# Kernel optimization log

Hardware: AMD Instinct MI355X
Metric: run time of the kernel (lower is better)

## Reference

```python
import jax, jax.numpy as jnp
import numpy as np
from jax import lax

T, Nn, K, IN, H1, H2, G, P, HEADS = 64, 2048, 32, 256, 128, 128, 256, 60, 3


def setup_inputs() -> dict:
    key = jax.random.key(0)
    ks = jax.random.split(key, 20)
    s = 0.05  # weight scale to keep activations sane
    return {
        'h': jax.random.normal(ks[0], (T, Nn, IN), jnp.float32),
        'neigh': jax.random.randint(ks[1], (Nn, K), 0, Nn),
        'Npop': jnp.ones((1,), jnp.float32) * 1e6,
        'I': jax.random.uniform(ks[2], (T,), jnp.float32) * 1e4,
        'R': jax.random.uniform(ks[3], (T,), jnp.float32) * 1e4,
        'S': jax.random.uniform(ks[4], (T,), jnp.float32) * 9e5,
        'It': jax.random.uniform(ks[5], (T,), jnp.float32),
        'Rt': jax.random.uniform(ks[6], (T,), jnp.float32),
        'fc1': jax.random.normal(ks[7], (HEADS, IN, H1), jnp.float32) * s,
        'fc2': jax.random.normal(ks[8], (HEADS * H1, H2), jnp.float32) * s,
        'gru_Wih': jax.random.normal(ks[9], (3 * G, H2), jnp.float32) * s,
        'gru_Whh': jax.random.normal(ks[10], (3 * G, G), jnp.float32) * s,
        'gru_bih': jax.random.normal(ks[11], (3 * G,), jnp.float32) * s,
        'gru_bhh': jax.random.normal(ks[12], (3 * G,), jnp.float32) * s,
        'res1_W': jax.random.normal(ks[13], (2 * P, G + 2), jnp.float32) * s,
        'res1_b': jax.random.normal(ks[14], (2 * P,), jnp.float32) * s,
        'res2_W': jax.random.normal(ks[15], (2, G + 2), jnp.float32) * s,
        'res2_b': jax.random.normal(ks[16], (2,), jnp.float32) * s,
        'hx0': jax.random.normal(ks[17], (G,), jnp.float32),
    }


def _input_attention(iz, neigh):
    # cosine^4 edge scores, unnormalized weighted sum of neighbor feats
    src = iz[neigh]                                  # [N,K,d]
    dot = jnp.einsum('nkd,nd->nk', src, iz)
    nsrc = jnp.sqrt(jnp.einsum('nkd,nkd->nk', src, src))
    ndst = jnp.sqrt(jnp.sum(iz * iz, axis=-1))[:, None]
    e = (dot / nsrc / ndst) ** 4                     # [N,K]
    return jnp.einsum('nk,nkd->nd', e, src)


def _gat_head(x, W, neigh):
    # dot-product edge attention + per-node softmax + weighted reduce
    z = x @ W                                        # [N,H]
    src = z[neigh]                                   # [N,K,H]
    e = jnp.einsum('nkd,nd->nk', src, z)             # [N,K]
    a = jax.nn.softmax(e, axis=1)
    return jnp.einsum('nk,nkd->nd', a, src)


def _gru_cell(x, hx, Wih, Whh, bih, bhh):
    gi = Wih @ x + bih                               # [3G]
    gh = Whh @ hx + bhh
    ir, iz, inn = jnp.split(gi, 3)
    hr, hz, hn = jnp.split(gh, 3)
    r = jax.nn.sigmoid(ir + hr)
    zg = jax.nn.sigmoid(iz + hz)
    n = jnp.tanh(inn + r * hn)
    return (1.0 - zg) * n + zg * hx


def reference(h, neigh, Npop, I, R, S, It, Rt, fc1, fc2, gru_Wih, gru_Whh,
              gru_bih, gru_bhh, res1_W, res1_b, res2_W, res2_b, hx0):
    Np = Npop[0]

    def step(hx, xs):
        h_t, I_t, R_t, S_t, It_t, Rt_t = xs
        ih = _input_attention(h_t, neigh)                       # [N,in]
        heads = jax.vmap(lambda W: _gat_head(ih, W, neigh))(fc1)  # [3,N,H1]
        c = jax.nn.relu(jnp.transpose(heads, (1, 0, 2)).reshape(Nn, HEADS * H1))
        c = _gat_head(c, fc2, neigh)                            # [N,H2]
        pooled = jnp.max(jax.nn.relu(c), axis=0)                # [H2]
        hx = _gru_cell(pooled, hx, gru_Wih, gru_Whh, gru_bih, gru_bhh)
        nhx = jnp.concatenate([hx, It_t[None], Rt_t[None]])     # [G+2]
        pred = res1_W @ nhx + res1_b                            # [2P]
        ab = res2_W @ nhx + res2_b
        a_s = jax.nn.sigmoid(ab[0])
        b_s = jax.nn.sigmoid(ab[1])
        new_I = pred[0::2]
        new_R = pred[1::2]

        def sir(st, _):
            lI, lR, lS = st
            dI = a_s * lI * (lS / Np) - b_s * lI
            dR = b_s * lI
            nI = lI + lax.stop_gradient(dI)
            nR = lR + lax.stop_gradient(dR)
            nS = Np - nI - nR
            return (nI, nR, nS), (dI, dR)

        _, (pI, pR) = lax.scan(sir, (I_t, R_t, S_t), None, length=P)
        return hx, (new_I, new_R, pI, pR)

    _, (new_I, new_R, phy_I, phy_R) = lax.scan(step, hx0, (h, I, R, S, It, Rt))
    return (new_I, new_R, phy_I.reshape(-1), phy_R.reshape(-1))
```

## Files before the change

### kernel.cpp

```cpp
#include <hip/hip_runtime.h>
#include <hip/hip_bf16.h>
#include <math.h>

#define T_STEPS 64
#define NN      2048
#define KN      32
#define IND     256
#define H1D     128
#define C1D     384
#define H2D     128
#define GD      256
#define PD      60
#define GRU_NB  8

#define BITREV5_INIT {0,16,8,24,4,20,12,28,2,18,10,26,6,22,14,30, \
                      1,17,9,25,5,21,13,29,3,19,11,27,7,23,15,31}

__device__ __forceinline__ float bcast_lane(float v, int lane_imm) {
    return __uint_as_float(__builtin_amdgcn_readlane(__float_as_uint(v), lane_imm));
}

__device__ __forceinline__ float xpose_reduce16(float part[16], int lane) {
#pragma unroll
    for (int i = 0; i < 8; ++i) {
        float send = (lane & 2) ? part[i] : part[i + 8];
        float keep = (lane & 2) ? part[i + 8] : part[i];
        part[i] = keep + __shfl_xor(send, 2);
    }
#pragma unroll
    for (int i = 0; i < 4; ++i) {
        float send = (lane & 4) ? part[i] : part[i + 4];
        float keep = (lane & 4) ? part[i + 4] : part[i];
        part[i] = keep + __shfl_xor(send, 4);
    }
#pragma unroll
    for (int i = 0; i < 2; ++i) {
        float send = (lane & 8) ? part[i] : part[i + 2];
        float keep = (lane & 8) ? part[i + 2] : part[i];
        part[i] = keep + __shfl_xor(send, 8);
    }
    {
        float send = (lane & 16) ? part[0] : part[1];
        float keep = (lane & 16) ? part[1] : part[0];
        part[0] = keep + __shfl_xor(send, 16);
    }
    return part[0] + __shfl_xor(part[0], 32);
}

__global__ __launch_bounds__(256) void norms_kernel(const float* __restrict__ h,
                                                    float* __restrict__ norms,
                                                    int t_base) {
    int gw   = (int)((blockIdx.x * blockDim.x + threadIdx.x) >> 6);
    int lane = threadIdx.x & 63;
    int n    = gw & (NN - 1);
    int tloc = gw >> 11;
    const float4* row = (const float4*)(h + ((size_t)(t_base + tloc) * NN + n) * IND);
    float4 v = row[lane];
    float s = v.x * v.x + v.y * v.y + v.z * v.z + v.w * v.w;
#pragma unroll
    for (int off = 32; off > 0; off >>= 1) s += __shfl_xor(s, off);
    if (lane == 0) norms[(size_t)tloc * NN + n] = sqrtf(s);
}

__global__ __launch_bounds__(256, 4) void input_attn_kernel(const float* __restrict__ h,
                                                            const int* __restrict__ neigh,
                                                            const float* __restrict__ norms,
                                                            float* __restrict__ ih,
                                                            int t_base) {
    const int BR[32] = BITREV5_INIT;
    __shared__ float hd_s[2][2][32];
    int wave    = threadIdx.x >> 6;
    int nodeloc = wave >> 1;
    int half    = wave & 1;
    int lane    = threadIdx.x & 63;
    int gw   = (int)((blockIdx.x << 1) | nodeloc);
    int n    = gw & (NN - 1);
    int tloc = gw >> 11;
    const float* hT  = h + (size_t)(t_base + tloc) * NN * IND;
    const float* nrm = norms + (size_t)tloc * NN;

    const float2* dst2 = (const float2*)(hT + (size_t)n * IND + half * 128);
    float2 d = dst2[lane];

    int   jreg = neigh[n * KN + (lane & 31)];
    float nj   = nrm[jreg];
    float ndst = nrm[n];

    float2 rr[32];
    float comb[16];
#pragma unroll
    for (int i = 0; i < 16; ++i) {
        int sja = __builtin_amdgcn_readlane(jreg, BR[i]);
        int sjb = __builtin_amdgcn_readlane(jreg, BR[i + 16]);
        const float2* sa = (const float2*)(hT + (size_t)sja * IND + half * 128);
        const float2* sb = (const float2*)(hT + (size_t)sjb * IND + half * 128);
        rr[i]      = sa[lane];
        rr[i + 16] = sb[lane];
        float pa = rr[i].x * d.x + rr[i].y * d.y;
        float pb = rr[i + 16].x * d.x + rr[i + 16].y * d.y;
        float send = (lane & 1) ? pa : pb;
        float keep = (lane & 1) ? pb : pa;
        comb[i] = keep + __shfl_xor(send, 1);
    }
#pragma unroll
    for (int i = 0; i < 32; ++i) asm volatile("" : "+v"(rr[i].x), "+v"(rr[i].y));
    float hdot = xpose_reduce16(comb, lane);
    if (lane < 32) hd_s[nodeloc][half][lane] = hdot;
    __syncthreads();
    float dot = hdot + hd_s[nodeloc][half ^ 1][lane & 31];

    float r  = dot / (nj * ndst);
    float r2 = r * r;
    float e  = r2 * r2;

    float a0 = 0.f, a1 = 0.f;
#pragma unroll
    for (int i = 0; i < 32; ++i) {
        float ek = bcast_lane(e, BR[i]);
        a0 += ek * rr[i].x;
        a1 += ek * rr[i].y;
    }
    float2* orow = (float2*)(ih + (size_t)gw * IND + half * 128);
    orow[lane] = make_float2(a0, a1);
}

__global__ __launch_bounds__(256) void matmul_f32(const float* __restrict__ A,
                                                  const float* __restrict__ B,
                                                  float* __restrict__ C,
                                                  int M, int N, int K) {
    __shared__ float As[16][65];
    __shared__ float Bs[16][68];
    int tid  = threadIdx.x;
    int row0 = blockIdx.y * 64;
    int col0 = blockIdx.x * 64;
    int tr = tid >> 4, tc = tid & 15;
    float acc[4][4] = {};
    int la_m = tid >> 2;
    int la_k = (tid & 3) * 4;
    int lb_k = tid >> 4;
    int lb_n = (tid & 15) * 4;
    for (int k0 = 0; k0 < K; k0 += 16) {
        float4 av = *(const float4*)(A + (size_t)(row0 + la_m) * K + k0 + la_k);
        float4 bv = *(const float4*)(B + (size_t)(k0 + lb_k) * N + col0 + lb_n);
        __syncthreads();
        As[la_k + 0][la_m] = av.x; As[la_k + 1][la_m] = av.y;
        As[la_k + 2][la_m] = av.z; As[la_k + 3][la_m] = av.w;
        *(float4*)&Bs[lb_k][lb_n] = bv;
        __syncthreads();
#pragma unroll
        for (int kk = 0; kk < 16; ++kk) {
            float a[4], b[4];
#pragma unroll
            for (int r = 0; r < 4; ++r) a[r] = As[kk][tr * 4 + r];
#pragma unroll
            for (int c = 0; c < 4; ++c) b[c] = Bs[kk][tc * 4 + c];
#pragma unroll
            for (int r = 0; r < 4; ++r)
#pragma unroll
                for (int c = 0; c < 4; ++c) acc[r][c] += a[r] * b[c];
        }
    }
#pragma unroll
    for (int r = 0; r < 4; ++r) {
        float4 v = { acc[r][0], acc[r][1], acc[r][2], acc[r][3] };
        *(float4*)(C + (size_t)(row0 + tr * 4 + r) * N + col0 + tc * 4) = v;
    }
}

__global__ __launch_bounds__(192, 4) void gat_heads_kernel(const float* __restrict__ z1,
                                                           const int* __restrict__ neigh,
                                                           float* __restrict__ c) {
    const int BR[32] = BITREV5_INIT;
    int n    = blockIdx.x & (NN - 1);
    const float* ztbl = z1 + (size_t)(blockIdx.x >> 11) * NN * C1D;
    int head = threadIdx.x >> 6;
    int lane = threadIdx.x & 63;

    const float2* dst2 = (const float2*)(ztbl + (size_t)n * C1D + head * H1D);
    float2 d = dst2[lane];
    int jreg = neigh[n * KN + (lane & 31)];

    float2 rr[32];
    float comb[16];
#pragma unroll
    for (int i = 0; i < 16; ++i) {
        int sja = __builtin_amdgcn_readlane(jreg, BR[i]);
        int sjb = __builtin_amdgcn_readlane(jreg, BR[i + 16]);
        const float2* sa = (const float2*)(ztbl + (size_t)sja * C1D + head * H1D);
        const float2* sb = (const float2*)(ztbl + (size_t)sjb * C1D + head * H1D);
        rr[i]      = sa[lane];
        rr[i + 16] = sb[lane];
        float pa = rr[i].x * d.x + rr[i].y * d.y;
        float pb = rr[i + 16].x * d.x + rr[i + 16].y * d.y;
        float send = (lane & 1) ? pa : pb;
        float keep = (lane & 1) ? pb : pa;
        comb[i] = keep + __shfl_xor(send, 1);
    }
#pragma unroll
    for (int i = 0; i < 32; ++i) asm volatile("" : "+v"(rr[i].x), "+v"(rr[i].y));
    float dot = xpose_reduce16(comb, lane);

    float m = dot;
#pragma unroll
    for (int off = 16; off > 0; off >>= 1) m = fmaxf(m, __shfl_xor(m, off));
    float p = __expf(dot - m);
    float s = p;
#pragma unroll
    for (int off = 16; off > 0; off >>= 1) s += __shfl_xor(s, off);
    p /= s;

    float a0 = 0.f, a1 = 0.f;
#pragma unroll
    for (int i = 0; i < 32; ++i) {
        float pk = bcast_lane(p, BR[i]);
        a0 += pk * rr[i].x;
        a1 += pk * rr[i].y;
    }
    float2* orow = (float2*)(c + (size_t)blockIdx.x * C1D + (size_t)head * H1D);
    orow[lane] = make_float2(fmaxf(a0, 0.f), fmaxf(a1, 0.f));
}

__global__ __launch_bounds__(256, 4) void gat_final_kernel(const float* __restrict__ z2,
                                                           const int* __restrict__ neigh,
                                                           float* __restrict__ pooled,
                                                           int t_base) {
    const int BR[32] = BITREV5_INIT;
    __shared__ float2 red_s[4][64];
    int wave = threadIdx.x >> 6;
    int gw   = (int)((blockIdx.x << 2) | wave);
    int n    = gw & (NN - 1);
    int tloc = gw >> 11;
    const float* ztbl = z2 + (size_t)tloc * NN * H2D;
    int lane = threadIdx.x & 63;

    const float2* dst2 = (const float2*)(ztbl + (size_t)n * H2D);
    float2 d = dst2[lane];
    int jreg = neigh[n * KN + (lane & 31)];

    float2 rr[32];
    float comb[16];
#pragma unroll
    for (int i = 0; i < 16; ++i) {
        int sja = __builtin_amdgcn_readlane(jreg, BR[i]);
        int sjb = __builtin_amdgcn_readlane(jreg, BR[i + 16]);
        const float2* sa = (const float2*)(ztbl + (size_t)sja * H2D);
        const float2* sb = (const float2*)(ztbl + (size_t)sjb * H2D);
        rr[i]      = sa[lane];
        rr[i + 16] = sb[lane];
        float pa = rr[i].x * d.x + rr[i].y * d.y;
        float pb = rr[i + 16].x * d.x + rr[i + 16].y * d.y;
        float send = (lane & 1) ? pa : pb;
        float keep = (lane & 1) ? pb : pa;
        comb[i] = keep + __shfl_xor(send, 1);
    }
#pragma unroll
    for (int i = 0; i < 32; ++i) asm volatile("" : "+v"(rr[i].x), "+v"(rr[i].y));
    float dot = xpose_reduce16(comb, lane);

    float m = dot;
#pragma unroll
    for (int off = 16; off > 0; off >>= 1) m = fmaxf(m, __shfl_xor(m, off));
    float p = __expf(dot - m);
    float s = p;
#pragma unroll
    for (int off = 16; off > 0; off >>= 1) s += __shfl_xor(s, off);
    p /= s;

    float a0 = 0.f, a1 = 0.f;
#pragma unroll
    for (int i = 0; i < 32; ++i) {
        float pk = bcast_lane(p, BR[i]);
        a0 += pk * rr[i].x;
        a1 += pk * rr[i].y;
    }
    red_s[wave][lane] = make_float2(fmaxf(a0, 0.f), fmaxf(a1, 0.f));
    __syncthreads();
    if (wave == 0) {
        float mx0 = red_s[0][lane].x, mx1 = red_s[0][lane].y;
#pragma unroll
        for (int q = 1; q < 4; ++q) {
            mx0 = fmaxf(mx0, red_s[q][lane].x);
            mx1 = fmaxf(mx1, red_s[q][lane].y);
        }
        int* dst = (int*)(pooled + (size_t)(t_base + tloc) * H2D + lane * 2);
        atomicMax(dst,     __float_as_int(mx0));
        atomicMax(dst + 1, __float_as_int(mx1));
    }
}

__global__ void prep_W1(const float* __restrict__ fc1, float* __restrict__ W1,
                        unsigned int* __restrict__ cnt,
                        float* __restrict__ pooled) {
    int i = blockIdx.x * 256 + threadIdx.x;
    if (i < 256 * 384) {
        int d = i / 384, cf = i % 384;
        int hd = cf >> 7, j = cf & 127;
        W1[i] = fc1[(size_t)hd * 256 * 128 + (size_t)d * 128 + j];
    }
    if (i < T_STEPS) cnt[i] = 0u;
    if (i < T_STEPS * H2D) pooled[i] = 0.f;
}

__global__ __launch_bounds__(256) void gi_all_kernel(const float* __restrict__ Wih,
                                                     const float* __restrict__ bih,
                                                     const float* __restrict__ pooled,
                                                     float* __restrict__ gi_all) {
    __shared__ float p_s[H2D];
    int t  = blockIdx.x / 3;
    int ob = (blockIdx.x % 3) * 256;
    if (threadIdx.x < H2D) p_s[threadIdx.x] = pooled[t * H2D + threadIdx.x];
    __syncthreads();
    int o = ob + threadIdx.x;
    float acc = bih[o];
    const float* wr = Wih + (size_t)o * H2D;
#pragma unroll 4
    for (int d = 0; d < H2D; ++d) acc += wr[d] * p_s[d];
    gi_all[t * 768 + o] = acc;
}

__global__ __launch_bounds__(768) void gru_reg_kernel(const float* __restrict__ Whh,
                                                      const float* __restrict__ bhh,
                                                      const float* __restrict__ gi_all,
                                                      const float* __restrict__ hx0,
                                                      float* hx_all,
                                                      unsigned int* cnt) {
    __shared__ float4 hx_pad[72];
    __shared__ __align__(16) float hx_lin[GD];
    __shared__ float gh_s[96];
    int b   = blockIdx.x;
    int tid = threadIdx.x;
    int row_local = tid >> 3;
    int sub       = tid & 7;
    int chunk     = row_local >> 5;
    int r_in      = row_local & 31;
    int grow      = chunk * GD + b * 32 + r_in;

    float4 wreg[8];
    const float4* wrow = (const float4*)(Whh + (size_t)grow * GD + sub * 32);
#pragma unroll
    for (int i = 0; i < 8; ++i) wreg[i] = wrow[i];
    float bias = (sub == 0) ? bhh[grow] : 0.f;

    for (int t = 0; t < T_STEPS; ++t) {
        if (t > 0) {
            if (tid == 0) {
                while (__hip_atomic_load(&cnt[t - 1], __ATOMIC_ACQUIRE,
                                         __HIP_MEMORY_SCOPE_AGENT) < GRU_NB)
                    __builtin_amdgcn_s_sleep(1);
            }
            __syncthreads();
        }
        const float* hsrc = (t == 0) ? hx0 : (hx_all + (size_t)(t - 1) * GD);
        if (tid < 64) {
            float4 v;
            v.x = __hip_atomic_load(hsrc + tid * 4 + 0, __ATOMIC_RELAXED, __HIP_MEMORY_SCOPE_AGENT);
            v.y = __hip_atomic_load(hsrc + tid * 4 + 1, __ATOMIC_RELAXED, __HIP_MEMORY_SCOPE_AGENT);
            v.z = __hip_atomic_load(hsrc + tid * 4 + 2, __ATOMIC_RELAXED, __HIP_MEMORY_SCOPE_AGENT);
            v.w = __hip_atomic_load(hsrc + tid * 4 + 3, __ATOMIC_RELAXED, __HIP_MEMORY_SCOPE_AGENT);
            hx_pad[(tid >> 3) * 9 + (tid & 7)] = v;
            ((float4*)hx_lin)[tid] = v;
        }
        __syncthreads();

        float acc = 0.f;
#pragma unroll
        for (int i = 0; i < 8; ++i) {
            float4 hv = hx_pad[sub * 9 + i];
            float4 wv = wreg[i];
            acc += wv.x * hv.x + wv.y * hv.y + wv.z * hv.z + wv.w * hv.w;
        }
        acc += __shfl_xor(acc, 1);
        acc += __shfl_xor(acc, 2);
        acc += __shfl_xor(acc, 4);
        if (sub == 0) gh_s[row_local] = acc + bias;
        __syncthreads();

        if (tid < 32) {
            int u = b * 32 + tid;
            float gi_r = gi_all[t * 768 + u];
            float gi_z = gi_all[t * 768 + 256 + u];
            float gi_n = gi_all[t * 768 + 512 + u];
            float r  = 1.f / (1.f + expf(-(gi_r + gh_s[tid])));
            float zg = 1.f / (1.f + expf(-(gi_z + gh_s[32 + tid])));
            float nn = tanhf(gi_n + r * gh_s[64 + tid]);
            float hnew = (1.f - zg) * nn + zg * hx_lin[u];
            __hip_atomic_store(&hx_all[(size_t)t * GD + u], hnew,
                               __ATOMIC_RELAXED, __HIP_MEMORY_SCOPE_AGENT);
            __threadfence();
        }
        __syncthreads();
        if (tid == 0)
            __hip_atomic_fetch_add(&cnt[t], 1u, __ATOMIC_RELEASE,
                                   __HIP_MEMORY_SCOPE_AGENT);
    }
}

__global__ __launch_bounds__(128) void res_sir_kernel(const float* __restrict__ hx_all,
                                                      const float* __restrict__ It,
                                                      const float* __restrict__ Rt,
                                                      const float* __restrict__ r1W,
                                                      const float* __restrict__ r1b,
                                                      const float* __restrict__ r2W,
                                                      const float* __restrict__ r2b,
                                                      const float* __restrict__ I,
                                                      const float* __restrict__ R,
                                                      const float* __restrict__ S,
                                                      const float* __restrict__ Npop,
                                                      float* __restrict__ out) {
    __shared__ float nhx[258];
    __shared__ float ab_s[2];
    int t = blockIdx.x, tid = threadIdx.x;
    for (int i = tid; i < GD; i += 128) nhx[i] = hx_all[t * GD + i];
    if (tid == 0) { nhx[256] = It[t]; nhx[257] = Rt[t]; }
    __syncthreads();
    if (tid < 120) {
        float acc = r1b[tid];
        const float* wr = r1W + tid * 258;
        for (int d = 0; d < 258; ++d) acc += wr[d] * nhx[d];
        int idx = t * 60 + (tid >> 1);
        if (tid & 1) out[3840 + idx] = acc;
        else         out[idx] = acc;
    }
    if (tid == 120 || tid == 121) {
        int q = tid - 120;
        float acc = r2b[q];
        const float* wr = r2W + q * 258;
        for (int d = 0; d < 258; ++d) acc += wr[d] * nhx[d];
        ab_s[q] = acc;
    }
    __syncthreads();
    if (tid == 0) {
        float a_s = 1.f / (1.f + expf(-ab_s[0]));
        float b_s = 1.f / (1.f + expf(-ab_s[1]));
        float Np = Npop[0];
        float lI = I[t], lR = R[t], lS = S[t];
        for (int p = 0; p < PD; ++p) {
            float dI = a_s * lI * (lS / Np) - b_s * lI;
            float dR = b_s * lI;
            lI += dI;
            lR += dR;
            lS = Np - lI - lR;
            out[7680  + t * 60 + p] = dI;
            out[11520 + t * 60 + p] = dR;
        }
    }
}

extern "C" void kernel_launch(void* const* d_in, const int* in_sizes, int n_in,
                              void* d_out, int out_size, void* d_ws, size_t ws_size,
                              hipStream_t stream) {
    const float* h    = (const float*)d_in[0];
    const int*   ng   = (const int*)  d_in[1];
    const float* Npop = (const float*)d_in[2];
    const float* I_   = (const float*)d_in[3];
    const float* R_   = (const float*)d_in[4];
    const float* S_   = (const float*)d_in[5];
    const float* It   = (const float*)d_in[6];
    const float* Rt   = (const float*)d_in[7];
    const float* fc1  = (const float*)d_in[8];
    const float* fc2  = (const float*)d_in[9];
    const float* gWih = (const float*)d_in[10];
    const float* gWhh = (const float*)d_in[11];
    const float* gbih = (const float*)d_in[12];
    const float* gbhh = (const float*)d_in[13];
    const float* r1W  = (const float*)d_in[14];
    const float* r1b  = (const float*)d_in[15];
    const float* r2W  = (const float*)d_in[16];
    const float* r2b  = (const float*)d_in[17];
    const float* hx0  = (const float*)d_in[18];
    float* out = (float*)d_out;

    char* w = (char*)d_ws;
    float* pooled = (float*)w; w += (size_t)T_STEPS * H2D * 4;
    float* hx_all = (float*)w; w += (size_t)T_STEPS * GD * 4;
    float* W1     = (float*)w; w += (size_t)256 * 384 * 4;
    float* gi_all = (float*)w; w += (size_t)T_STEPS * 768 * 4;
    unsigned int* cnt = (unsigned int*)w; w += 256;
    size_t fixed = (size_t)(w - (char*)d_ws);

    int Tc = 16;
    while (Tc > 1) {
        size_t need = fixed + (size_t)Tc * (8192 + 2ull * 2048 * 384 * 4);
        if (need <= ws_size) break;
        Tc >>= 1;
    }
    float* norms = (float*)w; w += (size_t)Tc * NN * 4;
    float* bufA  = (float*)w; w += (size_t)Tc * NN * C1D * 4;
    float* bufB  = (float*)w;

    prep_W1<<<(256 * 384 + 255) / 256, 256, 0, stream>>>(fc1, W1, cnt, pooled);

    for (int t0 = 0; t0 < T_STEPS; t0 += Tc) {
        int M = Tc * NN;
        norms_kernel      <<<Tc * NN / 4, 256, 0, stream>>>(h, norms, t0);
        input_attn_kernel <<<Tc * NN / 2, 256, 0, stream>>>(h, ng, norms, bufA, t0);
        matmul_f32<<<dim3(384 / 64, M / 64), 256, 0, stream>>>(bufA, W1, bufB, M, 384, 256);
        gat_heads_kernel  <<<Tc * NN, 192, 0, stream>>>(bufB, ng, bufA);
        matmul_f32<<<dim3(128 / 64, M / 64), 256, 0, stream>>>(bufA, fc2, bufB, M, 128, 384);
        gat_final_kernel  <<<Tc * NN / 4, 256, 0, stream>>>(bufB, ng, pooled, t0);
    }

    gi_all_kernel<<<T_STEPS * 3, 256, 0, stream>>>(gWih, gbih, pooled, gi_all);
    gru_reg_kernel<<<GRU_NB, 768, 0, stream>>>(gWhh, gbhh, gi_all, hx0, hx_all, cnt);
    res_sir_kernel<<<T_STEPS, 128, 0, stream>>>(hx_all, It, Rt, r1W, r1b, r2W, r2b,
                                                I_, R_, S_, Npop, out);
}
```

Before: 1.774 ms.

## Replace atomic max pooling with two-stage reduction and batch gather loads

```diff
diff --git a/kernel.cpp b/kernel.cpp
--- a/kernel.cpp
+++ b/kernel.cpp
@@ -87,23 +87,23 @@
     float ndst = nrm[n];
 
     float2 rr[32];
+#pragma unroll
+    for (int i = 0; i < 32; ++i) {
+        int sj = __builtin_amdgcn_readlane(jreg, BR[i]);
+        rr[i] = ((const float2*)(hT + (size_t)sj * IND + half * 128))[lane];
+    }
+#pragma unroll
+    for (int i = 0; i < 32; ++i) asm volatile("" : "+v"(rr[i].x), "+v"(rr[i].y));
+
     float comb[16];
 #pragma unroll
     for (int i = 0; i < 16; ++i) {
-        int sja = __builtin_amdgcn_readlane(jreg, BR[i]);
-        int sjb = __builtin_amdgcn_readlane(jreg, BR[i + 16]);
-        const float2* sa = (const float2*)(hT + (size_t)sja * IND + half * 128);
-        const float2* sb = (const float2*)(hT + (size_t)sjb * IND + half * 128);
-        rr[i]      = sa[lane];
-        rr[i + 16] = sb[lane];
         float pa = rr[i].x * d.x + rr[i].y * d.y;
         float pb = rr[i + 16].x * d.x + rr[i + 16].y * d.y;
         float send = (lane & 1) ? pa : pb;
         float keep = (lane & 1) ? pb : pa;
         comb[i] = keep + __shfl_xor(send, 1);
     }
-#pragma unroll
-    for (int i = 0; i < 32; ++i) asm volatile("" : "+v"(rr[i].x), "+v"(rr[i].y));
     float hdot = xpose_reduce16(comb, lane);
     if (lane < 32) hd_s[nodeloc][half][lane] = hdot;
     __syncthreads();
@@ -181,23 +181,23 @@
     int jreg = neigh[n * KN + (lane & 31)];
 
     float2 rr[32];
+#pragma unroll
+    for (int i = 0; i < 32; ++i) {
+        int sj = __builtin_amdgcn_readlane(jreg, BR[i]);
+        rr[i] = ((const float2*)(ztbl + (size_t)sj * C1D + head * H1D))[lane];
+    }
+#pragma unroll
+    for (int i = 0; i < 32; ++i) asm volatile("" : "+v"(rr[i].x), "+v"(rr[i].y));
+
     float comb[16];
 #pragma unroll
     for (int i = 0; i < 16; ++i) {
-        int sja = __builtin_amdgcn_readlane(jreg, BR[i]);
-        int sjb = __builtin_amdgcn_readlane(jreg, BR[i + 16]);
-        const float2* sa = (const float2*)(ztbl + (size_t)sja * C1D + head * H1D);
-        const float2* sb = (const float2*)(ztbl + (size_t)sjb * C1D + head * H1D);
-        rr[i]      = sa[lane];
-        rr[i + 16] = sb[lane];
         float pa = rr[i].x * d.x + rr[i].y * d.y;
         float pb = rr[i + 16].x * d.x + rr[i + 16].y * d.y;
         float send = (lane & 1) ? pa : pb;
         float keep = (lane & 1) ? pb : pa;
         comb[i] = keep + __shfl_xor(send, 1);
     }
-#pragma unroll
-    for (int i = 0; i < 32; ++i) asm volatile("" : "+v"(rr[i].x), "+v"(rr[i].y));
     float dot = xpose_reduce16(comb, lane);
 
     float m = dot;
@@ -222,15 +222,11 @@
 
 __global__ __launch_bounds__(256, 4) void gat_final_kernel(const float* __restrict__ z2,
                                                            const int* __restrict__ neigh,
-                                                           float* __restrict__ pooled,
-                                                           int t_base) {
+                                                           float* __restrict__ c2) {
     const int BR[32] = BITREV5_INIT;
-    __shared__ float2 red_s[4][64];
-    int wave = threadIdx.x >> 6;
-    int gw   = (int)((blockIdx.x << 2) | wave);
+    int gw   = (int)((blockIdx.x << 2) | (threadIdx.x >> 6));
     int n    = gw & (NN - 1);
-    int tloc = gw >> 11;
-    const float* ztbl = z2 + (size_t)tloc * NN * H2D;
+    const float* ztbl = z2 + (size_t)(gw >> 11) * NN * H2D;
     int lane = threadIdx.x & 63;
 
     const float2* dst2 = (const float2*)(ztbl + (size_t)n * H2D);
@@ -238,23 +234,23 @@
     int jreg = neigh[n * KN + (lane & 31)];
 
     float2 rr[32];
+#pragma unroll
+    for (int i = 0; i < 32; ++i) {
+        int sj = __builtin_amdgcn_readlane(jreg, BR[i]);
+        rr[i] = ((const float2*)(ztbl + (size_t)sj * H2D))[lane];
+    }
+#pragma unroll
+    for (int i = 0; i < 32; ++i) asm volatile("" : "+v"(rr[i].x), "+v"(rr[i].y));
+
     float comb[16];
 #pragma unroll
     for (int i = 0; i < 16; ++i) {
-        int sja = __builtin_amdgcn_readlane(jreg, BR[i]);
-        int sjb = __builtin_amdgcn_readlane(jreg, BR[i + 16]);
-        const float2* sa = (const float2*)(ztbl + (size_t)sja * H2D);
-        const float2* sb = (const float2*)(ztbl + (size_t)sjb * H2D);
-        rr[i]      = sa[lane];
-        rr[i + 16] = sb[lane];
         float pa = rr[i].x * d.x + rr[i].y * d.y;
         float pb = rr[i + 16].x * d.x + rr[i + 16].y * d.y;
         float send = (lane & 1) ? pa : pb;
         float keep = (lane & 1) ? pb : pa;
         comb[i] = keep + __shfl_xor(send, 1);
     }
-#pragma unroll
-    for (int i = 0; i < 32; ++i) asm volatile("" : "+v"(rr[i].x), "+v"(rr[i].y));
     float dot = xpose_reduce16(comb, lane);
 
     float m = dot;
@@ -273,24 +269,33 @@
         a0 += pk * rr[i].x;
         a1 += pk * rr[i].y;
     }
-    red_s[wave][lane] = make_float2(fmaxf(a0, 0.f), fmaxf(a1, 0.f));
-    __syncthreads();
-    if (wave == 0) {
-        float mx0 = red_s[0][lane].x, mx1 = red_s[0][lane].y;
-#pragma unroll
-        for (int q = 1; q < 4; ++q) {
-            mx0 = fmaxf(mx0, red_s[q][lane].x);
-            mx1 = fmaxf(mx1, red_s[q][lane].y);
-        }
-        int* dst = (int*)(pooled + (size_t)(t_base + tloc) * H2D + lane * 2);
-        atomicMax(dst,     __float_as_int(mx0));
-        atomicMax(dst + 1, __float_as_int(mx1));
-    }
+    float2* orow = (float2*)(c2 + (size_t)gw * H2D);
+    orow[lane] = make_float2(fmaxf(a0, 0.f), fmaxf(a1, 0.f));
+}
+
+__global__ __launch_bounds__(128) void pool_part_kernel(const float* __restrict__ c2,
+                                                        float* __restrict__ ppart) {
+    int j = threadIdx.x;
+    int tloc  = blockIdx.x >> 4;
+    int slice = blockIdx.x & 15;
+    const float* base = c2 + ((size_t)tloc * NN + slice * 128) * H2D;
+    float mx = 0.f;
+    for (int q = 0; q < 128; ++q) mx = fmaxf(mx, base[(size_t)q * H2D + j]);
+    ppart[(size_t)blockIdx.x * H2D + j] = mx;
+}
+__global__ __launch_bounds__(128) void pool_reduce_kernel(const float* __restrict__ ppart,
+                                                          float* __restrict__ pooled,
+                                                          int t_base) {
+    int j = threadIdx.x;
+    const float* base = ppart + (size_t)blockIdx.x * 16 * H2D;
+    float mx = 0.f;
+#pragma unroll
+    for (int q = 0; q < 16; ++q) mx = fmaxf(mx, base[(size_t)q * H2D + j]);
+    pooled[(t_base + blockIdx.x) * H2D + j] = mx;
 }
 
 __global__ void prep_W1(const float* __restrict__ fc1, float* __restrict__ W1,
-                        unsigned int* __restrict__ cnt,
-                        float* __restrict__ pooled) {
+                        unsigned int* __restrict__ cnt) {
     int i = blockIdx.x * 256 + threadIdx.x;
     if (i < 256 * 384) {
         int d = i / 384, cf = i % 384;
@@ -298,7 +303,6 @@
         W1[i] = fc1[(size_t)hd * 256 * 128 + (size_t)d * 128 + j];
     }
     if (i < T_STEPS) cnt[i] = 0u;
-    if (i < T_STEPS * H2D) pooled[i] = 0.f;
 }
 
 __global__ __launch_bounds__(256) void gi_all_kernel(const float* __restrict__ Wih,
@@ -386,7 +390,6 @@
             float hnew = (1.f - zg) * nn + zg * hx_lin[u];
             __hip_atomic_store(&hx_all[(size_t)t * GD + u], hnew,
                                __ATOMIC_RELAXED, __HIP_MEMORY_SCOPE_AGENT);
-            __threadfence();
         }
         __syncthreads();
         if (tid == 0)
@@ -475,6 +478,7 @@
     float* hx_all = (float*)w; w += (size_t)T_STEPS * GD * 4;
     float* W1     = (float*)w; w += (size_t)256 * 384 * 4;
     float* gi_all = (float*)w; w += (size_t)T_STEPS * 768 * 4;
+    float* ppart  = (float*)w; w += (size_t)T_STEPS * 16 * H2D * 4;
     unsigned int* cnt = (unsigned int*)w; w += 256;
     size_t fixed = (size_t)(w - (char*)d_ws);
 
@@ -488,7 +492,7 @@
     float* bufA  = (float*)w; w += (size_t)Tc * NN * C1D * 4;
     float* bufB  = (float*)w;
 
-    prep_W1<<<(256 * 384 + 255) / 256, 256, 0, stream>>>(fc1, W1, cnt, pooled);
+    prep_W1<<<(256 * 384 + 255) / 256, 256, 0, stream>>>(fc1, W1, cnt);
 
     for (int t0 = 0; t0 < T_STEPS; t0 += Tc) {
         int M = Tc * NN;
@@ -497,7 +501,9 @@
         matmul_f32<<<dim3(384 / 64, M / 64), 256, 0, stream>>>(bufA, W1, bufB, M, 384, 256);
         gat_heads_kernel  <<<Tc * NN, 192, 0, stream>>>(bufB, ng, bufA);
         matmul_f32<<<dim3(128 / 64, M / 64), 256, 0, stream>>>(bufA, fc2, bufB, M, 128, 384);
-        gat_final_kernel  <<<Tc * NN / 4, 256, 0, stream>>>(bufB, ng, pooled, t0);
+        gat_final_kernel  <<<Tc * NN / 4, 256, 0, stream>>>(bufB, ng, bufA);
+        pool_part_kernel  <<<Tc * 16, 128, 0, stream>>>(bufA, ppart);
+        pool_reduce_kernel<<<Tc, 128, 0, stream>>>(ppart, pooled, t0);
     }
 
     gi_all_kernel<<<T_STEPS * 3, 256, 0, stream>>>(gWih, gbih, pooled, gi_all);
```

Result: no change. 1.778 ms (+0.3%).
